# Kernel optimization log

Measured on AMD Instinct MI355X. Metric: run time of the kernel, lower is better.

Reference implementation:

```python
import jax, jax.numpy as jnp
import numpy as np

N = 100000      # nodes
E = 1600000     # edges
F_IN = 27       # node features
EMB = 64        # embedding size
H = 128         # hidden/out channels
L = 4           # GNN layers
G = 512         # num_graphs


def setup_inputs() -> dict:
    key = jax.random.key(0)
    ks = jax.random.split(key, 13)
    s = 0.05
    return {
        "x": jax.random.normal(ks[0], (N, F_IN), jnp.float32),
        "edge_index": jax.random.randint(ks[1], (2, E), 0, N),
        "batch": jnp.sort(jax.random.randint(ks[2], (N,), 0, G)),
        "lin0_w": jax.random.normal(ks[3], (F_IN, EMB), jnp.float32) * s,
        "ggc_weight": jax.random.normal(ks[4], (L, H, H), jnp.float32) * s,
        "gru_w_ih": jax.random.normal(ks[5], (3 * H, H), jnp.float32) * s,
        "gru_w_hh": jax.random.normal(ks[6], (3 * H, H), jnp.float32) * s,
        "gru_b_ih": jax.random.normal(ks[7], (3 * H,), jnp.float32) * s,
        "gru_b_hh": jax.random.normal(ks[8], (3 * H,), jnp.float32) * s,
        "lin1_w": jax.random.normal(ks[9], (H, 1), jnp.float32) * s,
        "lin1_b": jax.random.normal(ks[10], (1,), jnp.float32) * s,
        "lin2_w": jax.random.normal(ks[11], (H, 1), jnp.float32) * s,
        "lin2_b": jax.random.normal(ks[12], (1,), jnp.float32) * s,
    }


def _gru_cell(m, h, w_ih, w_hh, b_ih, b_hh):
    # torch.nn.GRUCell math
    gi = m @ w_ih.T + b_ih          # [N, 3H]
    gh = h @ w_hh.T + b_hh          # [N, 3H]
    i_r, i_z, i_n = jnp.split(gi, 3, axis=1)
    h_r, h_z, h_n = jnp.split(gh, 3, axis=1)
    r = jax.nn.sigmoid(i_r + h_r)
    z = jax.nn.sigmoid(i_z + h_z)
    n = jnp.tanh(i_n + r * h_n)
    return (1.0 - z) * n + z * h


def reference(x, edge_index, batch, lin0_w, ggc_weight,
              gru_w_ih, gru_w_hh, gru_b_ih, gru_b_hh,
              lin1_w, lin1_b, lin2_w, lin2_b):
    x1 = jax.nn.sigmoid(x @ lin0_w)                       # [N, EMB]
    h = jnp.pad(x1, ((0, 0), (0, H - EMB)))               # pad to out_channels
    src, dst = edge_index[0], edge_index[1]
    for i in range(L):
        m = h @ ggc_weight[i]                             # [N, H]
        m = jax.ops.segment_sum(m[src], dst, num_segments=N)  # add-aggregate at target
        h = _gru_cell(m, h, gru_w_ih, gru_w_hh, gru_b_ih, gru_b_hh)
    xr = jax.nn.relu(h)
    mu = xr @ lin1_w + lin1_b                             # [N, 1]
    sigma = jax.nn.softplus(xr @ lin2_w + lin2_b)         # [N, 1]
    uncorrected_mu = mu
    mu_all = jax.ops.segment_sum(mu, batch, num_segments=G)        # [G, 1]
    sigma_all = jax.ops.segment_sum(sigma, batch, num_segments=G)  # [G, 1]
    # vectorized per-graph correction (original loops over graphs)
    mu_c = mu - mu_all[batch] * (sigma / sigma_all[batch])
    return (mu_c.squeeze(1), x1, sigma.squeeze(1), uncorrected_mu.squeeze(1))
```

## Files before the change

### kernel.cpp

```cpp
#include <hip/hip_runtime.h>
#include <math.h>

#define NN 100000
#define FIN 27
#define EMB 64
#define HH 128
#define LAYERS 4
#define GG 512
#define SCAN_CHUNK 2048
#define SPAN 512
#define SPANSHIFT 9
#define MAXNB 256
#define ECAP 16384
#define LPAD_US 136
#define TM 64

typedef __attribute__((ext_vector_type(8))) short short8;
typedef __attribute__((ext_vector_type(4))) float floatx4;

__device__ __forceinline__ float sigmf(float x) { return 1.0f / (1.0f + __expf(-x)); }
__device__ __forceinline__ float tanhfast(float x) { return 1.0f - 2.0f / (__expf(2.0f * x) + 1.0f); }

__device__ __forceinline__ unsigned short f2bf(float f) {
    unsigned int u = __float_as_uint(f);
    u += 0x7FFFu + ((u >> 16) & 1u);
    return (unsigned short)(u >> 16);
}

__device__ __forceinline__ float bflo(unsigned int v) { return __uint_as_float(v << 16); }
__device__ __forceinline__ float bfhi(unsigned int v) { return __uint_as_float(v & 0xFFFF0000u); }
__device__ __forceinline__ float bfs(unsigned short v) { return __uint_as_float(((unsigned)v) << 16); }

__global__ void lin0_kernel(const float* __restrict__ x, const float* __restrict__ w,
                            float* __restrict__ x1_out, unsigned short* __restrict__ hbf, int n) {
    int wave = (int)((blockIdx.x * blockDim.x + threadIdx.x) >> 6);
    int lane = threadIdx.x & 63;
    if (wave >= n) return;
    const float* xr = x + (size_t)wave * FIN;
    float acc = 0.0f;
#pragma unroll
    for (int k = 0; k < FIN; ++k) acc += xr[k] * w[k * EMB + lane];
    float v = 1.0f / (1.0f + expf(-acc));
    x1_out[(size_t)wave * EMB + lane] = v;
    hbf[(size_t)wave * HH + lane] = f2bf(v);
}

__global__ void bucket_scatter_direct(const int* __restrict__ src, const int* __restrict__ dst,
                                      int* __restrict__ bucket_cnt, unsigned* __restrict__ ebuf,
                                      int e) {
    __shared__ int lh[MAXNB];
    __shared__ int gb[MAXNB];
    int t = threadIdx.x;
    for (int i = t; i < MAXNB; i += 1024) lh[i] = 0;
    __syncthreads();
    int base = blockIdx.x * 16384;
    int lidx[16], sv[16], dv[16];
#pragma unroll
    for (int i = 0; i < 16; ++i) {
        int eid = base + i * 1024 + t;
        if (eid < e) {
            sv[i] = src[eid];
            dv[i] = dst[eid];
            lidx[i] = atomicAdd(&lh[dv[i] >> SPANSHIFT], 1);
        } else lidx[i] = -1;
    }
    __syncthreads();
    for (int i = t; i < MAXNB; i += 1024) {
        int c = lh[i];
        gb[i] = c ? atomicAdd(&bucket_cnt[i], c) : 0;
    }
    __syncthreads();
#pragma unroll
    for (int i = 0; i < 16; ++i) {
        if (lidx[i] >= 0) {
            int b = dv[i] >> SPANSHIFT;
            int pos = gb[b] + lidx[i];
            if (pos < ECAP) {
                unsigned dl = (unsigned)(dv[i] - (b << SPANSHIFT));
                ebuf[(size_t)b * ECAP + pos] = (dl << 17) | (unsigned)sv[i];
            }
        }
    }
}

__global__ void deg_from_buckets(const unsigned* __restrict__ ebuf, const int* __restrict__ bucket_cnt,
                                 int* __restrict__ deg, int n) {
    __shared__ int ld[SPAN];
    int b = blockIdx.x, t = threadIdx.x;
    ld[t] = 0; ld[t + 256] = 0;
    __syncthreads();
    int cnt = bucket_cnt[b];
    if (cnt > ECAP) cnt = ECAP;
    size_t base = (size_t)b * ECAP;
    int nodebase = b << SPANSHIFT;
    for (int j = t; j < cnt; j += 256)
        atomicAdd(&ld[ebuf[base + j] >> 17], 1);
    __syncthreads();
    int i0 = nodebase + t, i1 = nodebase + 256 + t;
    if (i0 < n) deg[i0] = ld[t];
    if (i1 < n) deg[i1] = ld[t + 256];
}

__global__ void scan_partial(const int* __restrict__ deg, int* __restrict__ blocksum, int n) {
    int b = blockIdx.x, t = threadIdx.x;
    int base = b * SCAN_CHUNK + t * 8;
    int s = 0;
#pragma unroll
    for (int i = 0; i < 8; ++i) {
        int idx = base + i;
        if (idx < n) s += deg[idx];
    }
#pragma unroll
    for (int off = 32; off > 0; off >>= 1) s += __shfl_down(s, off, 64);
    __shared__ int ws[4];
    if ((t & 63) == 0) ws[t >> 6] = s;
    __syncthreads();
    if (t == 0) blocksum[b] = ws[0] + ws[1] + ws[2] + ws[3];
}

__global__ void scan_blocksums(const int* __restrict__ blocksum, int* __restrict__ blockoff, int nb) {
    int t = threadIdx.x;
    int own = (t < nb) ? blocksum[t] : 0;
    int v = own;
    for (int off = 1; off < 64; off <<= 1) {
        int u = __shfl_up(v, off, 64);
        if (t >= off) v += u;
    }
    if (t < nb) blockoff[t] = v - own;
}

__global__ void scan_final(const int* __restrict__ deg, const int* __restrict__ blockoff,
                           int* __restrict__ rowptr, int n) {
    int b = blockIdx.x, t = threadIdx.x;
    int base = b * SCAN_CHUNK + t * 8;
    int v[8];
    int s = 0;
#pragma unroll
    for (int i = 0; i < 8; ++i) {
        int idx = base + i;
        v[i] = (idx < n) ? deg[idx] : 0;
        s += v[i];
    }
    __shared__ int ts[256];
    ts[t] = s;
    __syncthreads();
    for (int off = 1; off < 256; off <<= 1) {
        int u = (t >= off) ? ts[t - off] : 0;
        __syncthreads();
        ts[t] += u;
        __syncthreads();
    }
    int run = blockoff[b] + ((t == 0) ? 0 : ts[t - 1]);
#pragma unroll
    for (int i = 0; i < 8; ++i) {
        int idx = base + i;
        if (idx < n) {
            rowptr[idx] = run;
            run += v[i];
        } else if (idx == n) {
            rowptr[n] = run;
        }
    }
}

__global__ void place_kernel(const unsigned* __restrict__ ebuf, const int* __restrict__ bucket_cnt,
                             const int* __restrict__ rowptr, int* __restrict__ col, int n) {
    __shared__ int cur[SPAN];
    int b = blockIdx.x, t = threadIdx.x;
    int nodebase = b << SPANSHIFT;
    int i0 = nodebase + t, i1 = nodebase + 256 + t;
    cur[t] = (i0 < n) ? rowptr[i0] : 0;
    cur[t + 256] = (i1 < n) ? rowptr[i1] : 0;
    __syncthreads();
    int cnt = bucket_cnt[b];
    if (cnt > ECAP) cnt = ECAP;
    size_t base = (size_t)b * ECAP;
    for (int j = t; j < cnt; j += 256) {
        unsigned ed = ebuf[base + j];
        int pos = atomicAdd(&cur[ed >> 17], 1);
        col[pos] = (int)(ed & 0x1FFFFu);
    }
}

template <int HALF>
__global__ __launch_bounds__(512, 8)
void agg_kernel(const unsigned short* __restrict__ hin, unsigned short* __restrict__ aggout,
                const int* __restrict__ rowptr, const int* __restrict__ col, int n) {
    int node = (int)((blockIdx.x * blockDim.x + threadIdx.x) >> 6);
    int lane = threadIdx.x & 63;
    if (node >= n) return;
    int l16 = lane & 15;
    int lg = lane >> 4;
    const uint4* hin4 = (const uint4*)hin;
    const uint2* hin2 = (const uint2*)hin;
    int r0 = rowptr[node];
    int r1 = rowptr[node + 1];

    if (HALF) {
        float a[4], b[4];
#pragma unroll
        for (int k = 0; k < 4; ++k) { a[k] = 0.0f; b[k] = 0.0f; }
        int j = r0 + lg;
        for (; j + 4 < r1; j += 8) {
            int s0 = col[j], s1 = col[j + 4];
            uint2 v0 = hin2[(size_t)s0 * 32 + l16];
            uint2 v1 = hin2[(size_t)s1 * 32 + l16];
            a[0] += bflo(v0.x); a[1] += bfhi(v0.x);
            a[2] += bflo(v0.y); a[3] += bfhi(v0.y);
            b[0] += bflo(v1.x); b[1] += bfhi(v1.x);
            b[2] += bflo(v1.y); b[3] += bfhi(v1.y);
        }
        for (; j < r1; j += 4) {
            int s = col[j];
            uint2 v = hin2[(size_t)s * 32 + l16];
            a[0] += bflo(v.x); a[1] += bfhi(v.x);
            a[2] += bflo(v.y); a[3] += bfhi(v.y);
        }
#pragma unroll
        for (int k = 0; k < 4; ++k) {
            a[k] += b[k];
            a[k] += __shfl_xor(a[k], 32, 64);
            a[k] += __shfl_xor(a[k], 16, 64);
        }
        if (lg == 0) {
            uint2 o;
            o.x = (unsigned)f2bf(a[0]) | ((unsigned)f2bf(a[1]) << 16);
            o.y = (unsigned)f2bf(a[2]) | ((unsigned)f2bf(a[3]) << 16);
            *(uint2*)(aggout + (size_t)node * HH + l16 * 4) = o;
        }
    } else {
        float a[8], b[8];
#pragma unroll
        for (int k = 0; k < 8; ++k) { a[k] = 0.0f; b[k] = 0.0f; }
        int j = r0 + lg;
        for (; j + 12 < r1; j += 16) {
            int s0 = col[j], s1 = col[j + 4], s2 = col[j + 8], s3 = col[j + 12];
            uint4 v0 = hin4[(size_t)s0 * 16 + l16];
            uint4 v1 = hin4[(size_t)s1 * 16 + l16];
            uint4 v2 = hin4[(size_t)s2 * 16 + l16];
            uint4 v3 = hin4[(size_t)s3 * 16 + l16];
            a[0] += bflo(v0.x); a[1] += bfhi(v0.x);
            a[2] += bflo(v0.y); a[3] += bfhi(v0.y);
            a[4] += bflo(v0.z); a[5] += bfhi(v0.z);
            a[6] += bflo(v0.w); a[7] += bfhi(v0.w);
            b[0] += bflo(v1.x); b[1] += bfhi(v1.x);
            b[2] += bflo(v1.y); b[3] += bfhi(v1.y);
            b[4] += bflo(v1.z); b[5] += bfhi(v1.z);
            b[6] += bflo(v1.w); b[7] += bfhi(v1.w);
            a[0] += bflo(v2.x); a[1] += bfhi(v2.x);
            a[2] += bflo(v2.y); a[3] += bfhi(v2.y);
            a[4] += bflo(v2.z); a[5] += bfhi(v2.z);
            a[6] += bflo(v2.w); a[7] += bfhi(v2.w);
            b[0] += bflo(v3.x); b[1] += bfhi(v3.x);
            b[2] += bflo(v3.y); b[3] += bfhi(v3.y);
            b[4] += bflo(v3.z); b[5] += bfhi(v3.z);
            b[6] += bflo(v3.w); b[7] += bfhi(v3.w);
        }
        for (; j + 4 < r1; j += 8) {
            int s0 = col[j], s1 = col[j + 4];
            uint4 v0 = hin4[(size_t)s0 * 16 + l16];
            uint4 v1 = hin4[(size_t)s1 * 16 + l16];
            a[0] += bflo(v0.x); a[1] += bfhi(v0.x);
            a[2] += bflo(v0.y); a[3] += bfhi(v0.y);
            a[4] += bflo(v0.z); a[5] += bfhi(v0.z);
            a[6] += bflo(v0.w); a[7] += bfhi(v0.w);
            b[0] += bflo(v1.x); b[1] += bfhi(v1.x);
            b[2] += bflo(v1.y); b[3] += bfhi(v1.y);
            b[4] += bflo(v1.z); b[5] += bfhi(v1.z);
            b[6] += bflo(v1.w); b[7] += bfhi(v1.w);
        }
        for (; j < r1; j += 4) {
            int s = col[j];
            uint4 v = hin4[(size_t)s * 16 + l16];
            a[0] += bflo(v.x); a[1] += bfhi(v.x);
            a[2] += bflo(v.y); a[3] += bfhi(v.y);
            a[4] += bflo(v.z); a[5] += bfhi(v.z);
            a[6] += bflo(v.w); a[7] += bfhi(v.w);
        }
#pragma unroll
        for (int k = 0; k < 8; ++k) {
            a[k] += b[k];
            a[k] += __shfl_xor(a[k], 32, 64);
            a[k] += __shfl_xor(a[k], 16, 64);
        }
        if (lg == 0) {
            uint4 o;
            o.x = (unsigned)f2bf(a[0]) | ((unsigned)f2bf(a[1]) << 16);
            o.y = (unsigned)f2bf(a[2]) | ((unsigned)f2bf(a[3]) << 16);
            o.z = (unsigned)f2bf(a[4]) | ((unsigned)f2bf(a[5]) << 16);
            o.w = (unsigned)f2bf(a[6]) | ((unsigned)f2bf(a[7]) << 16);
            *(uint4*)(aggout + (size_t)node * HH + l16 * 8) = o;
        }
    }
}

template <int HALF>
__global__ __launch_bounds__(512, 2)
void gru_kernel(const unsigned short* __restrict__ aggin,
                const unsigned short* __restrict__ hin,
                unsigned short* __restrict__ hout,
                const unsigned short* __restrict__ Wfp,
                const unsigned short* __restrict__ whhp,
                const float* __restrict__ b_ih, const float* __restrict__ b_hh,
                int n) {
    __shared__ unsigned short aggL[TM * LPAD_US];
    __shared__ unsigned short hL[TM * LPAD_US];
    int wave = threadIdx.x >> 6;
    int lane = threadIdx.x & 63;
    int quad = lane >> 4;
    int l15 = lane & 15;
    int M0 = blockIdx.x * TM;
    if (M0 >= n) return;

#pragma unroll
    for (int i = 0; i < 2; ++i) {
        int idx = threadIdx.x + i * 512;
        int row = idx >> 4;
        int q = idx & 15;
        int gr = M0 + row;
        uint4 va = make_uint4(0, 0, 0, 0), vh = va;
        if (gr < n && !(HALF && q >= 8)) {
            va = ((const uint4*)aggin)[(size_t)gr * 16 + q];
            vh = ((const uint4*)hin)[(size_t)gr * 16 + q];
        }
        *(uint4*)(&aggL[row * LPAD_US + q * 8]) = va;
        *(uint4*)(&hL[row * LPAD_US + q * 8]) = vh;
    }
    __syncthreads();

    floatx4 gi[4][3], gh[4][3];
#pragma unroll
    for (int m = 0; m < 4; ++m)
#pragma unroll
        for (int g = 0; g < 3; ++g) {
            gi[m][g] = (floatx4)0.0f;
            gh[m][g] = (floatx4)0.0f;
        }

    const int KTMAX = HALF ? 2 : 4;
#pragma unroll
    for (int kt = 0; kt < KTMAX; ++kt) {
        int kbase = kt * 32 + quad * 8;
        short8 aA[4], aH[4];
#pragma unroll
        for (int m = 0; m < 4; ++m) {
            aA[m] = *(const short8*)(&aggL[(m * 16 + l15) * LPAD_US + kbase]);
            aH[m] = *(const short8*)(&hL[(m * 16 + l15) * LPAD_US + kbase]);
        }
#pragma unroll
        for (int g = 0; g < 3; ++g) {
            int ct = g * 8 + wave;
            size_t boff = ((size_t)(kt * 24 + ct) * 64 + lane) * 8;
            short8 bi = *(const short8*)(Wfp + boff);
            short8 bh = *(const short8*)(whhp + boff);
#pragma unroll
            for (int m = 0; m < 4; ++m) {
                gi[m][g] = __builtin_amdgcn_mfma_f32_16x16x32_bf16(aA[m], bi, gi[m][g], 0, 0, 0);
                gh[m][g] = __builtin_amdgcn_mfma_f32_16x16x32_bf16(aH[m], bh, gh[m][g], 0, 0, 0);
            }
        }
    }

    __syncthreads();

    {
        int c = wave * 16 + l15;
        float bir = b_ih[c], biz = b_ih[128 + c], bin_ = b_ih[256 + c];
        float bhr = b_hh[c], bhz = b_hh[128 + c], bhn = b_hh[256 + c];
#pragma unroll
        for (int m = 0; m < 4; ++m) {
#pragma unroll
            for (int j = 0; j < 4; ++j) {
                int row = m * 16 + quad * 4 + j;
                int lidx = row * LPAD_US + c;
                float gir = gi[m][0][j] + bir;
                float ghr = gh[m][0][j] + bhr;
                float giz = gi[m][1][j] + biz;
                float ghz = gh[m][1][j] + bhz;
                float gin = gi[m][2][j] + bin_;
                float ghn = gh[m][2][j] + bhn;
                float rr = sigmf(gir + ghr);
                float zz = sigmf(giz + ghz);
                float nn = tanhfast(gin + rr * ghn);
                float hp = bfs(hL[lidx]);
                aggL[lidx] = f2bf((1.0f - zz) * nn + zz * hp);
            }
        }
    }

    __syncthreads();

#pragma unroll
    for (int i = 0; i < 2; ++i) {
        int idx = threadIdx.x + i * 512;
        int row = idx >> 4;
        int q = idx & 15;
        int gr = M0 + row;
        if (gr < n) {
            uint4 v = *(const uint4*)(&aggL[row * LPAD_US + q * 8]);
            *(uint4*)(hout + (size_t)gr * HH + q * 8) = v;
        }
    }
}

__global__ void pack_whh(const float* __restrict__ w_hh, unsigned short* __restrict__ whhp) {
    int id = blockIdx.x * blockDim.x + threadIdx.x;
    if (id >= 4 * 24 * 64 * 8) return;
    int j = id & 7;
    int lane = (id >> 3) & 63;
    int ctkt = id >> 9;
    int ct = ctkt % 24;
    int kt = ctkt / 24;
    int k = kt * 32 + (lane >> 4) * 8 + j;
    int col = ct * 16 + (lane & 15);
    whhp[id] = f2bf(w_hh[col * HH + k]);
}

__global__ void pack_wf(const float* __restrict__ ggc, const float* __restrict__ w_ih,
                        unsigned short* __restrict__ Wfp) {
    int id = blockIdx.x * blockDim.x + threadIdx.x;
    if (id >= LAYERS * 4 * 24 * 64 * 8) return;
    int l = id / 49152;
    int rem = id % 49152;
    int j = rem & 7;
    int lane = (rem >> 3) & 63;
    int ctkt = rem >> 9;
    int ct = ctkt % 24;
    int kt = ctkt / 24;
    int k = kt * 32 + (lane >> 4) * 8 + j;
    int col = ct * 16 + (lane & 15);
    const float4* gr = (const float4*)(ggc + ((size_t)l * HH + k) * HH);
    const float4* wr = (const float4*)(w_ih + (size_t)col * HH);
    float acc = 0.0f;
#pragma unroll 4
    for (int q = 0; q < HH / 4; ++q) {
        float4 g = gr[q], w = wr[q];
        acc += g.x * w.x + g.y * w.y + g.z * w.z + g.w * w.w;
    }
    Wfp[id] = f2bf(acc);
}

__global__ void readout_kernel(const unsigned int* __restrict__ h2, const float* __restrict__ w1,
                               const float* __restrict__ b1, const float* __restrict__ w2,
                               const float* __restrict__ b2,
                               float* __restrict__ out_mu, float* __restrict__ out_sg, int n) {
    int wave = (int)((blockIdx.x * blockDim.x + threadIdx.x) >> 6);
    int lane = threadIdx.x & 63;
    if (wave >= n) return;
    unsigned int u = h2[(size_t)wave * 64 + lane];
    float x0 = fmaxf(bflo(u), 0.0f);
    float x1 = fmaxf(bfhi(u), 0.0f);
    float2 wv1 = ((const float2*)w1)[lane];
    float2 wv2 = ((const float2*)w2)[lane];
    float a1 = x0 * wv1.x + x1 * wv1.y;
    float a2 = x0 * wv2.x + x1 * wv2.y;
#pragma unroll
    for (int off = 32; off > 0; off >>= 1) {
        a1 += __shfl_down(a1, off, 64);
        a2 += __shfl_down(a2, off, 64);
    }
    if (lane == 0) {
        float mu = a1 + b1[0];
        float x2 = a2 + b2[0];
        float sg = (x2 > 20.0f) ? x2 : __logf(1.0f + __expf(x2));
        out_mu[wave] = mu;
        out_sg[wave] = sg;
    }
}

__device__ __forceinline__ int lbound(const int* __restrict__ a, int n, int v) {
    int lo = 0, hi = n;
    while (lo < hi) {
        int m = (lo + hi) >> 1;
        if (a[m] < v) lo = m + 1; else hi = m;
    }
    return lo;
}

__global__ void seg_correct_kernel(const float* __restrict__ out_mu, const float* __restrict__ out_sg,
                                   const int* __restrict__ batch, float* __restrict__ out_muc, int n) {
    int g = blockIdx.x;
    int lo = lbound(batch, n, g);
    int hi = lbound(batch, n, g + 1);
    float smu = 0.0f, ssg = 0.0f;
    for (int i = lo + threadIdx.x; i < hi; i += blockDim.x) {
        smu += out_mu[i];
        ssg += out_sg[i];
    }
#pragma unroll
    for (int off = 32; off > 0; off >>= 1) {
        smu += __shfl_down(smu, off, 64);
        ssg += __shfl_down(ssg, off, 64);
    }
    __shared__ float pm[4], ps[4];
    int wave = threadIdx.x >> 6;
    int lane = threadIdx.x & 63;
    if (lane == 0) { pm[wave] = smu; ps[wave] = ssg; }
    __syncthreads();
    float tot_mu = pm[0] + pm[1] + pm[2] + pm[3];
    float tot_sg = ps[0] + ps[1] + ps[2] + ps[3];
    for (int i = lo + threadIdx.x; i < hi; i += blockDim.x) {
        out_muc[i] = out_mu[i] - tot_mu * (out_sg[i] / tot_sg);
    }
}

extern "C" void kernel_launch(void* const* d_in, const int* in_sizes, int n_in,
                              void* d_out, int out_size, void* d_ws, size_t ws_size,
                              hipStream_t stream) {
    const float* x      = (const float*)d_in[0];
    const int*   ei     = (const int*)d_in[1];
    const int*   batch  = (const int*)d_in[2];
    const float* lin0_w = (const float*)d_in[3];
    const float* ggc    = (const float*)d_in[4];
    const float* w_ih   = (const float*)d_in[5];
    const float* w_hh   = (const float*)d_in[6];
    const float* b_ih   = (const float*)d_in[7];
    const float* b_hh   = (const float*)d_in[8];
    const float* l1w    = (const float*)d_in[9];
    const float* l1b    = (const float*)d_in[10];
    const float* l2w    = (const float*)d_in[11];
    const float* l2b    = (const float*)d_in[12];

    int n = in_sizes[0] / FIN;
    int e = in_sizes[1] / 2;
    const int* src = ei;
    const int* dstp = ei + e;

    float* out = (float*)d_out;
    float* out_muc = out;
    float* out_x1  = out + n;
    float* out_sg  = out + n + (size_t)n * EMB;
    float* out_mu  = out_sg + n;

    unsigned short* hbf0 = (unsigned short*)d_ws;
    unsigned short* hbf1 = hbf0 + (size_t)n * HH;
    unsigned short* Wfp  = hbf1 + (size_t)n * HH;
    unsigned short* whhp = Wfp + (size_t)LAYERS * 49152;
    int*            deg      = (int*)(whhp + 49152 + 8);
    int*            rowptr   = deg + n;
    int*            blocksum = rowptr + n + 1;
    int*            blockoff = blocksum + 64;
    int*            bucket_cnt = blockoff + 64;
    int*            col      = bucket_cnt + MAXNB;
    unsigned*       ebuf     = (unsigned*)hbf1;

    int nbuck = (n + SPAN - 1) >> SPANSHIFT;
    hipMemsetAsync(bucket_cnt, 0, MAXNB * sizeof(int), stream);

    int wave_blocks = (n * 64 + 255) / 256;
    lin0_kernel<<<wave_blocks, 256, 0, stream>>>(x, lin0_w, out_x1, hbf0, n);

    int eb = (e + 16383) / 16384;
    bucket_scatter_direct<<<eb, 1024, 0, stream>>>(src, dstp, bucket_cnt, ebuf, e);
    deg_from_buckets<<<nbuck, 256, 0, stream>>>(ebuf, bucket_cnt, deg, n);

    int nb = (n + SCAN_CHUNK) / SCAN_CHUNK;
    scan_partial<<<nb, 256, 0, stream>>>(deg, blocksum, n);
    scan_blocksums<<<1, 64, 0, stream>>>(blocksum, blockoff, nb);
    scan_final<<<nb, 256, 0, stream>>>(deg, blockoff, rowptr, n);

    place_kernel<<<nbuck, 256, 0, stream>>>(ebuf, bucket_cnt, rowptr, col, n);

    pack_whh<<<(49152 + 255) / 256, 256, 0, stream>>>(w_hh, whhp);
    pack_wf<<<(LAYERS * 49152 + 255) / 256, 256, 0, stream>>>(ggc, w_ih, Wfp);

    int node_wave_blocks = (n + 7) / 8;
    int gru_blocks = (n + TM - 1) / TM;
    unsigned short* hin = hbf0;
    unsigned short* hother = hbf1;
    for (int l = 0; l < LAYERS; ++l) {
        if (l == 0) {
            agg_kernel<1><<<node_wave_blocks, 512, 0, stream>>>(hin, hother, rowptr, col, n);
            gru_kernel<1><<<gru_blocks, 512, 0, stream>>>(hother, hin, hother,
                                                          Wfp, whhp, b_ih, b_hh, n);
        } else {
            agg_kernel<0><<<node_wave_blocks, 512, 0, stream>>>(hin, hother, rowptr, col, n);
            gru_kernel<0><<<gru_blocks, 512, 0, stream>>>(hother, hin, hother,
                                                          Wfp + (size_t)l * 49152, whhp,
                                                          b_ih, b_hh, n);
        }
        unsigned short* t = hin; hin = hother; hother = t;
    }

    readout_kernel<<<wave_blocks, 256, 0, stream>>>((const unsigned int*)hin, l1w, l1b, l2w, l2b,
                                                    out_mu, out_sg, n);
    seg_correct_kernel<<<GG, 256, 0, stream>>>(out_mu, out_sg, batch, out_muc, n);
}
```

Measured before the change: 667.6 us.

## Make GRU kernel persistent with register-resident weights and direct global operands

The GRU kernel becomes a persistent grid of 256 blocks that stride over 64-row tiles. Each wave loads its W_ih and W_hh fragments into registers once instead of once per tile. The A operands are read directly from global memory instead of being staged through LDS, and results are written straight to global as individual bf16 values. The aim is to stop refetching weights for every tile and to drop the LDS round trips. In exchange, register pressure rises sharply, with weights and accumulators together near the launch-bound limit and a risk of spills. Output stores become narrow, partially coalesced writes, and only one block per CU is resident to hide latency.

```diff
diff --git a/kernel.cpp b/kernel.cpp
--- a/kernel.cpp
+++ b/kernel.cpp
@@ -12,7 +12,6 @@
 #define SPANSHIFT 9
 #define MAXNB 256
 #define ECAP 16384
-#define LPAD_US 136
 #define TM 64
 
 typedef __attribute__((ext_vector_type(8))) short short8;
@@ -302,103 +301,86 @@
                 const unsigned short* __restrict__ Wfp,
                 const unsigned short* __restrict__ whhp,
                 const float* __restrict__ b_ih, const float* __restrict__ b_hh,
-                int n) {
-    __shared__ unsigned short aggL[TM * LPAD_US];
-    __shared__ unsigned short hL[TM * LPAD_US];
+                int n, int nsteps) {
     int wave = threadIdx.x >> 6;
     int lane = threadIdx.x & 63;
     int quad = lane >> 4;
     int l15 = lane & 15;
-    int M0 = blockIdx.x * TM;
-    if (M0 >= n) return;
-
-#pragma unroll
-    for (int i = 0; i < 2; ++i) {
-        int idx = threadIdx.x + i * 512;
-        int row = idx >> 4;
-        int q = idx & 15;
-        int gr = M0 + row;
-        uint4 va = make_uint4(0, 0, 0, 0), vh = va;
-        if (gr < n && !(HALF && q >= 8)) {
-            va = ((const uint4*)aggin)[(size_t)gr * 16 + q];
-            vh = ((const uint4*)hin)[(size_t)gr * 16 + q];
-        }
-        *(uint4*)(&aggL[row * LPAD_US + q * 8]) = va;
-        *(uint4*)(&hL[row * LPAD_US + q * 8]) = vh;
-    }
-    __syncthreads();
-
-    floatx4 gi[4][3], gh[4][3];
-#pragma unroll
-    for (int m = 0; m < 4; ++m)
-#pragma unroll
-        for (int g = 0; g < 3; ++g) {
-            gi[m][g] = (floatx4)0.0f;
-            gh[m][g] = (floatx4)0.0f;
-        }
-
     const int KTMAX = HALF ? 2 : 4;
-#pragma unroll
-    for (int kt = 0; kt < KTMAX; ++kt) {
-        int kbase = kt * 32 + quad * 8;
-        short8 aA[4], aH[4];
+
+    short8 Bi[3][4], Bh[3][4];
+#pragma unroll
+    for (int g = 0; g < 3; ++g) {
+#pragma unroll
+        for (int kt = 0; kt < 4; ++kt) {
+            if (kt < KTMAX) {
+                int ct = g * 8 + wave;
+                size_t boff = ((size_t)(kt * 24 + ct) * 64 + lane) * 8;
+                Bi[g][kt] = *(const short8*)(Wfp + boff);
+                Bh[g][kt] = *(const short8*)(whhp + boff);
+            }
+        }
+    }
+
+    int c = wave * 16 + l15;
+    float bir = b_ih[c], biz = b_ih[128 + c], bin_ = b_ih[256 + c];
+    float bhr = b_hh[c], bhz = b_hh[128 + c], bhn = b_hh[256 + c];
+
+    for (int step = blockIdx.x; step < nsteps; step += gridDim.x) {
+        int M0 = step * TM;
+
+        floatx4 gi[4][3], gh[4][3];
+#pragma unroll
+        for (int m = 0; m < 4; ++m)
+#pragma unroll
+            for (int g = 0; g < 3; ++g) {
+                gi[m][g] = (floatx4)0.0f;
+                gh[m][g] = (floatx4)0.0f;
+            }
+
+        int rowA[4];
+#pragma unroll
+        for (int m = 0; m < 4; ++m) rowA[m] = min(M0 + m * 16 + l15, n - 1);
+
+#pragma unroll
+        for (int kt = 0; kt < 4; ++kt) {
+            if (kt < KTMAX) {
+                size_t ko = (size_t)kt * 32 + quad * 8;
+#pragma unroll
+                for (int m = 0; m < 4; ++m) {
+                    short8 aA = *(const short8*)(aggin + (size_t)rowA[m] * HH + ko);
+                    short8 aH = *(const short8*)(hin + (size_t)rowA[m] * HH + ko);
+#pragma unroll
+                    for (int g = 0; g < 3; ++g) {
+                        gi[m][g] = __builtin_amdgcn_mfma_f32_16x16x32_bf16(aA, Bi[g][kt], gi[m][g], 0, 0, 0);
+                        gh[m][g] = __builtin_amdgcn_mfma_f32_16x16x32_bf16(aH, Bh[g][kt], gh[m][g], 0, 0, 0);
+                    }
+                }
+            }
+        }
+
+        __syncthreads();
+
 #pragma unroll
         for (int m = 0; m < 4; ++m) {
-            aA[m] = *(const short8*)(&aggL[(m * 16 + l15) * LPAD_US + kbase]);
-            aH[m] = *(const short8*)(&hL[(m * 16 + l15) * LPAD_US + kbase]);
-        }
-#pragma unroll
-        for (int g = 0; g < 3; ++g) {
-            int ct = g * 8 + wave;
-            size_t boff = ((size_t)(kt * 24 + ct) * 64 + lane) * 8;
-            short8 bi = *(const short8*)(Wfp + boff);
-            short8 bh = *(const short8*)(whhp + boff);
-#pragma unroll
-            for (int m = 0; m < 4; ++m) {
-                gi[m][g] = __builtin_amdgcn_mfma_f32_16x16x32_bf16(aA[m], bi, gi[m][g], 0, 0, 0);
-                gh[m][g] = __builtin_amdgcn_mfma_f32_16x16x32_bf16(aH[m], bh, gh[m][g], 0, 0, 0);
+#pragma unroll
+            for (int j = 0; j < 4; ++j) {
+                int row = M0 + m * 16 + quad * 4 + j;
+                if (row < n) {
+                    float hp = 0.0f;
+                    if (!HALF || c < 64) hp = bfs(hin[(size_t)row * HH + c]);
+                    float gir = gi[m][0][j] + bir;
+                    float ghr = gh[m][0][j] + bhr;
+                    float giz = gi[m][1][j] + biz;
+                    float ghz = gh[m][1][j] + bhz;
+                    float gin = gi[m][2][j] + bin_;
+                    float ghn = gh[m][2][j] + bhn;
+                    float rr = sigmf(gir + ghr);
+                    float zz = sigmf(giz + ghz);
+                    float nnv = tanhfast(gin + rr * ghn);
+                    hout[(size_t)row * HH + c] = f2bf((1.0f - zz) * nnv + zz * hp);
+                }
             }
-        }
-    }
-
-    __syncthreads();
-
-    {
-        int c = wave * 16 + l15;
-        float bir = b_ih[c], biz = b_ih[128 + c], bin_ = b_ih[256 + c];
-        float bhr = b_hh[c], bhz = b_hh[128 + c], bhn = b_hh[256 + c];
-#pragma unroll
-        for (int m = 0; m < 4; ++m) {
-#pragma unroll
-            for (int j = 0; j < 4; ++j) {
-                int row = m * 16 + quad * 4 + j;
-                int lidx = row * LPAD_US + c;
-                float gir = gi[m][0][j] + bir;
-                float ghr = gh[m][0][j] + bhr;
-                float giz = gi[m][1][j] + biz;
-                float ghz = gh[m][1][j] + bhz;
-                float gin = gi[m][2][j] + bin_;
-                float ghn = gh[m][2][j] + bhn;
-                float rr = sigmf(gir + ghr);
-                float zz = sigmf(giz + ghz);
-                float nn = tanhfast(gin + rr * ghn);
-                float hp = bfs(hL[lidx]);
-                aggL[lidx] = f2bf((1.0f - zz) * nn + zz * hp);
-            }
-        }
-    }
-
-    __syncthreads();
-
-#pragma unroll
-    for (int i = 0; i < 2; ++i) {
-        int idx = threadIdx.x + i * 512;
-        int row = idx >> 4;
-        int q = idx & 15;
-        int gr = M0 + row;
-        if (gr < n) {
-            uint4 v = *(const uint4*)(&aggL[row * LPAD_US + q * 8]);
-            *(uint4*)(hout + (size_t)gr * HH + q * 8) = v;
         }
     }
 }
@@ -565,19 +547,19 @@
     pack_wf<<<(LAYERS * 49152 + 255) / 256, 256, 0, stream>>>(ggc, w_ih, Wfp);
 
     int node_wave_blocks = (n + 7) / 8;
-    int gru_blocks = (n + TM - 1) / TM;
+    int nsteps = (n + TM - 1) / TM;
     unsigned short* hin = hbf0;
     unsigned short* hother = hbf1;
     for (int l = 0; l < LAYERS; ++l) {
         if (l == 0) {
             agg_kernel<1><<<node_wave_blocks, 512, 0, stream>>>(hin, hother, rowptr, col, n);
-            gru_kernel<1><<<gru_blocks, 512, 0, stream>>>(hother, hin, hother,
-                                                          Wfp, whhp, b_ih, b_hh, n);
+            gru_kernel<1><<<256, 512, 0, stream>>>(hother, hin, hother,
+                                                   Wfp, whhp, b_ih, b_hh, n, nsteps);
         } else {
             agg_kernel<0><<<node_wave_blocks, 512, 0, stream>>>(hin, hother, rowptr, col, n);
-            gru_kernel<0><<<gru_blocks, 512, 0, stream>>>(hother, hin, hother,
-                                                          Wfp + (size_t)l * 49152, whhp,
-                                                          b_ih, b_hh, n);
+            gru_kernel<0><<<256, 512, 0, stream>>>(hother, hin, hother,
+                                                   Wfp + (size_t)l * 49152, whhp,
+                                                   b_ih, b_hh, n, nsteps);
         }
         unsigned short* t = hin; hin = hother; hother = t;
     }
```

Result: slower. 821.0 us (+23.0%).
